# Kernel tuning notes

Hardware: AMD Instinct MI355X
Metric: run time of the kernel (lower is better)

Reference implementation:

```python
import jax, jax.numpy as jnp
import numpy as np

NUM_NODES = 100000
NUM_EDGES = 6400000


def setup_inputs() -> dict:
    key = jax.random.key(0)
    k1, k2 = jax.random.split(key)
    e = jax.random.normal(k1, (NUM_EDGES,), dtype=jnp.float32)
    edge_index = jax.random.randint(k2, (2, NUM_EDGES), 0, NUM_NODES, dtype=jnp.int64 if jax.config.jax_enable_x64 else jnp.int32)
    return {"e": e, "edge_index": edge_index, "num_nodes": NUM_NODES}


def reference(e, edge_index, num_nodes):
    # GAT edge softmax (no max-subtraction, matching the 'simple' variant)
    target_nodes = edge_index[1]                      # [E]
    exp_e = jnp.exp(e)                                # [E]
    sum_exp = jax.ops.segment_sum(exp_e, target_nodes, num_segments=num_nodes)  # [N]
    alpha = exp_e / (sum_exp[target_nodes] + 1e-16)   # gather + normalize
    return alpha
```

## Files before the change

kernel.cpp:

```cpp
#include <hip/hip_runtime.h>


#define CHUNK 36864
#define SCAT_THREADS 1024
#define ASSUMED_N 100000
#define SUMS_RESERVE (1u << 20)


__global__ __launch_bounds__(SCAT_THREADS)
void gat_scatter_chunked(const float* __restrict__ e,
                         const int* __restrict__ tgt,
                         const int* __restrict__ np,
                         float* __restrict__ partials,
                         int per, int E, int Cmax) {
    __shared__ float hist[CHUNK];
    const int n = *np;
    int C = (n + CHUNK - 1) / CHUNK;
    if (C > Cmax) C = Cmax;

    const int b = blockIdx.x;
    const int start = b * per;
    const int end = min(start + per, E);
    const int len = (end > start) ? (end - start) : 0;
    const int vlen = len & ~3;

    for (int c = 0; c < C; ++c) {
        const int base = c * CHUNK;

        for (int i = threadIdx.x; i < CHUNK; i += SCAT_THREADS) hist[i] = 0.0f;
        __syncthreads();

        for (int i = threadIdx.x * 4; i < vlen; i += SCAT_THREADS * 4) {
            const float4 ev = *reinterpret_cast<const float4*>(e + start + i);
            const int4  tv = *reinterpret_cast<const int4*>(tgt + start + i);
            int t;
            t = tv.x - base; if ((unsigned)t < (unsigned)CHUNK) atomicAdd(&hist[t], __expf(ev.x));
            t = tv.y - base; if ((unsigned)t < (unsigned)CHUNK) atomicAdd(&hist[t], __expf(ev.y));
            t = tv.z - base; if ((unsigned)t < (unsigned)CHUNK) atomicAdd(&hist[t], __expf(ev.z));
            t = tv.w - base; if ((unsigned)t < (unsigned)CHUNK) atomicAdd(&hist[t], __expf(ev.w));
        }
        for (int i = vlen + threadIdx.x; i < len; i += SCAT_THREADS) {
            int t = tgt[start + i] - base;
            if ((unsigned)t < (unsigned)CHUNK) atomicAdd(&hist[t], __expf(e[start + i]));
        }
        __syncthreads();

        float* dst = partials + ((size_t)b * Cmax + c) * CHUNK;
        for (int i = threadIdx.x; i < CHUNK; i += SCAT_THREADS) dst[i] = hist[i];
        __syncthreads();
    }
}

__global__ void gat_reduce(const float* __restrict__ partials,
                           const int* __restrict__ np,
                           float* __restrict__ sums,
                           int B, int CC ) {
    const int n = *np;
    const int gs = gridDim.x * blockDim.x;
    for (int nd = blockIdx.x * blockDim.x + threadIdx.x; nd < n; nd += gs) {
        if (nd >= CC) { sums[nd] = 0.0f; continue; }
        const float* p = partials + nd;
        float s0 = 0.f, s1 = 0.f, s2 = 0.f, s3 = 0.f;
        int b = 0;
        for (; b + 3 < B; b += 4) {
            s0 += p[(size_t)(b + 0) * CC];
            s1 += p[(size_t)(b + 1) * CC];
            s2 += p[(size_t)(b + 2) * CC];
            s3 += p[(size_t)(b + 3) * CC];
        }
        for (; b < B; ++b) s0 += p[(size_t)b * CC];
        sums[nd] = (s0 + s1) + (s2 + s3);
    }
}


__global__ void gat_zero_sums(float* __restrict__ sums,
                              const int* __restrict__ np) {
    const int n = *np;
    const int stride = gridDim.x * blockDim.x;
    for (int i = blockIdx.x * blockDim.x + threadIdx.x; i < n; i += stride)
        sums[i] = 0.0f;
}

__global__ void gat_exp_scatter(const float4* __restrict__ e4,
                                const int4* __restrict__ t4,
                                const float* __restrict__ e,
                                const int* __restrict__ tgt,
                                float* __restrict__ sums,
                                int n4, int E) {
    const int stride = gridDim.x * blockDim.x;
    int tid = blockIdx.x * blockDim.x + threadIdx.x;
    for (int i = tid; i < n4; i += stride) {
        float4 ev = e4[i];
        int4 tv = t4[i];
        atomicAdd(&sums[tv.x], __expf(ev.x));
        atomicAdd(&sums[tv.y], __expf(ev.y));
        atomicAdd(&sums[tv.z], __expf(ev.z));
        atomicAdd(&sums[tv.w], __expf(ev.w));
    }
    const int tail_base = n4 * 4;
    const int tail_n = E - tail_base;
    if (tid < tail_n)
        atomicAdd(&sums[tgt[tail_base + tid]], __expf(e[tail_base + tid]));
}


__global__ void gat_normalize(const float4* __restrict__ e4,
                              const int4* __restrict__ t4,
                              const float* __restrict__ e,
                              const int* __restrict__ tgt,
                              const float* __restrict__ sums,
                              float4* __restrict__ out4,
                              float* __restrict__ out,
                              int n4, int E) {
    const int stride = gridDim.x * blockDim.x;
    int tid = blockIdx.x * blockDim.x + threadIdx.x;
    for (int i = tid; i < n4; i += stride) {
        float4 ev = e4[i];
        int4 tv = t4[i];
        float4 r;
        r.x = __expf(ev.x) / (sums[tv.x] + 1e-16f);
        r.y = __expf(ev.y) / (sums[tv.y] + 1e-16f);
        r.z = __expf(ev.z) / (sums[tv.z] + 1e-16f);
        r.w = __expf(ev.w) / (sums[tv.w] + 1e-16f);
        out4[i] = r;
    }
    const int tail_base = n4 * 4;
    const int tail_n = E - tail_base;
    if (tid < tail_n) {
        int i = tail_base + tid;
        out[i] = __expf(e[i]) / (sums[tgt[i]] + 1e-16f);
    }
}

extern "C" void kernel_launch(void* const* d_in, const int* in_sizes, int n_in,
                              void* d_out, int out_size, void* d_ws, size_t ws_size,
                              hipStream_t stream) {
    const float* e = (const float*)d_in[0];
    const int* edge_index = (const int*)d_in[1];
    const int* num_nodes_p = (const int*)d_in[2];

    const int E = in_sizes[0];
    const int* tgt = edge_index + E;

    float* sums = (float*)d_ws;
    float* alpha = (float*)d_out;
    const int n4 = E / 4;

    const int Cmax = (ASSUMED_N + CHUNK - 1) / CHUNK;

    int B = 256;
    while (B >= 32 &&
           (SUMS_RESERVE + (size_t)B * Cmax * CHUNK * sizeof(float)) > ws_size)
        B >>= 1;

    const bool use_chunked =
        (SUMS_RESERVE + (size_t)B * Cmax * CHUNK * sizeof(float)) <= ws_size;

    if (use_chunked) {
        float* partials = (float*)((char*)d_ws + SUMS_RESERVE);
        const int per = (((E + B - 1) / B) + 3) & ~3;

        gat_scatter_chunked<<<B, SCAT_THREADS, 0, stream>>>(
            e, tgt, num_nodes_p, partials, per, E, Cmax);

        gat_reduce<<<512, 256, 0, stream>>>(
            partials, num_nodes_p, sums, B, Cmax * CHUNK);
    } else {
        gat_zero_sums<<<512, 256, 0, stream>>>(sums, num_nodes_p);
        int blocks = (n4 + 255) / 256;
        if (blocks > 2048) blocks = 2048;
        if (blocks < 1) blocks = 1;
        gat_exp_scatter<<<blocks, 256, 0, stream>>>(
            (const float4*)e, (const int4*)tgt, e, tgt, sums, n4, E);
    }

    {
        int blocks = (n4 + 255) / 256;
        if (blocks > 2048) blocks = 2048;
        if (blocks < 1) blocks = 1;
        gat_normalize<<<blocks, 256, 0, stream>>>(
            (const float4*)e, (const int4*)tgt, e, tgt, sums,
            (float4*)alpha, alpha, n4, E);
    }
}
```

Measured before the change: 113.0 us.

## Cache edge data in registers across chunks and store bf16 partial histograms

The chunked scatter kernel now loads each block's edges and their exponentials into registers once, instead of re-reading e and tgt from global memory for every node chunk. Partial per-block histograms are written as packed bf16 rather than fp32, which halves partial-sum traffic in both scatter and reduce. The reduce is vectorized over four nodes per thread. The bf16 rounding loses precision in the partial sums, and register caching sharply raises register pressure under a tighter launch bound.

```diff
diff --git a/kernel.cpp b/kernel.cpp
--- a/kernel.cpp
+++ b/kernel.cpp
@@ -3,73 +3,133 @@
 
 #define CHUNK 36864
 #define SCAT_THREADS 1024
+#define NPT 7
 #define ASSUMED_N 100000
 #define SUMS_RESERVE (1u << 20)
 
-
-__global__ __launch_bounds__(SCAT_THREADS)
-void gat_scatter_chunked(const float* __restrict__ e,
-                         const int* __restrict__ tgt,
-                         const int* __restrict__ np,
-                         float* __restrict__ partials,
-                         int per, int E, int Cmax) {
+__device__ __forceinline__ unsigned bf16rne(float f) {
+    unsigned u = __float_as_uint(f);
+    return (u + 0x7FFFu + ((u >> 16) & 1u)) >> 16;
+}
+__device__ __forceinline__ float bf16tof(unsigned short h) {
+    return __uint_as_float(((unsigned)h) << 16);
+}
+
+
+__global__ __launch_bounds__(SCAT_THREADS, 4)
+void gat_scatter_regcache(const float* __restrict__ e,
+                          const int* __restrict__ tgt,
+                          const int* __restrict__ np,
+                          unsigned short* __restrict__ partials,
+                          int per, int E, int Cmax) {
     __shared__ float hist[CHUNK];
     const int n = *np;
     int C = (n + CHUNK - 1) / CHUNK;
     if (C > Cmax) C = Cmax;
 
     const int b = blockIdx.x;
-    const int start = b * per;
-    const int end = min(start + per, E);
-    const int len = (end > start) ? (end - start) : 0;
-    const int vlen = len & ~3;
+    const int tid = threadIdx.x;
+    const long long start = (long long)b * per;
+
+    int nv = per >> 2;
+    long long rem = (long long)E - start;
+    if (rem < 0) rem = 0;
+    if ((long long)nv > (rem >> 2)) nv = (int)(rem >> 2);
+    const int tail_lo = nv * 4;
+    int tail_hi = per;
+    if ((long long)tail_hi > rem) tail_hi = (int)rem;
+
+    const float4* e4 = reinterpret_cast<const float4*>(e + start);
+    const int4*  t4 = reinterpret_cast<const int4*>(tgt + start);
+
+    float4 xv[NPT];
+    int4   iv[NPT];
+#pragma unroll
+    for (int i = 0; i < NPT; ++i) {
+        const int v = i * SCAT_THREADS + tid;
+        if (v < nv) {
+            const float4 ev = e4[v];
+            iv[i] = t4[v];
+            xv[i].x = __expf(ev.x); xv[i].y = __expf(ev.y);
+            xv[i].z = __expf(ev.z); xv[i].w = __expf(ev.w);
+        } else {
+            iv[i].x = iv[i].y = iv[i].z = iv[i].w = -1;
+            xv[i].x = xv[i].y = xv[i].z = xv[i].w = 0.0f;
+        }
+    }
 
     for (int c = 0; c < C; ++c) {
         const int base = c * CHUNK;
 
-        for (int i = threadIdx.x; i < CHUNK; i += SCAT_THREADS) hist[i] = 0.0f;
+        float4 z; z.x = z.y = z.z = z.w = 0.0f;
+        for (int j = tid; j < (CHUNK / 4); j += SCAT_THREADS)
+            reinterpret_cast<float4*>(hist)[j] = z;
         __syncthreads();
 
-        for (int i = threadIdx.x * 4; i < vlen; i += SCAT_THREADS * 4) {
-            const float4 ev = *reinterpret_cast<const float4*>(e + start + i);
-            const int4  tv = *reinterpret_cast<const int4*>(tgt + start + i);
+#pragma unroll
+        for (int i = 0; i < NPT; ++i) {
             int t;
-            t = tv.x - base; if ((unsigned)t < (unsigned)CHUNK) atomicAdd(&hist[t], __expf(ev.x));
-            t = tv.y - base; if ((unsigned)t < (unsigned)CHUNK) atomicAdd(&hist[t], __expf(ev.y));
-            t = tv.z - base; if ((unsigned)t < (unsigned)CHUNK) atomicAdd(&hist[t], __expf(ev.z));
-            t = tv.w - base; if ((unsigned)t < (unsigned)CHUNK) atomicAdd(&hist[t], __expf(ev.w));
-        }
-        for (int i = vlen + threadIdx.x; i < len; i += SCAT_THREADS) {
+            t = iv[i].x - base; if ((unsigned)t < (unsigned)CHUNK) atomicAdd(&hist[t], xv[i].x);
+            t = iv[i].y - base; if ((unsigned)t < (unsigned)CHUNK) atomicAdd(&hist[t], xv[i].y);
+            t = iv[i].z - base; if ((unsigned)t < (unsigned)CHUNK) atomicAdd(&hist[t], xv[i].z);
+            t = iv[i].w - base; if ((unsigned)t < (unsigned)CHUNK) atomicAdd(&hist[t], xv[i].w);
+        }
+        for (int i = tail_lo + tid; i < tail_hi; i += SCAT_THREADS) {
             int t = tgt[start + i] - base;
             if ((unsigned)t < (unsigned)CHUNK) atomicAdd(&hist[t], __expf(e[start + i]));
         }
         __syncthreads();
 
-        float* dst = partials + ((size_t)b * Cmax + c) * CHUNK;
-        for (int i = threadIdx.x; i < CHUNK; i += SCAT_THREADS) dst[i] = hist[i];
+        unsigned* dst = reinterpret_cast<unsigned*>(
+            partials + ((size_t)b * Cmax + c) * CHUNK);
+        const float2* h2 = reinterpret_cast<const float2*>(hist);
+        for (int j = tid; j < (CHUNK / 2); j += SCAT_THREADS) {
+            const float2 hv = h2[j];
+            dst[j] = bf16rne(hv.x) | (bf16rne(hv.y) << 16);
+        }
         __syncthreads();
     }
 }
 
-__global__ void gat_reduce(const float* __restrict__ partials,
-                           const int* __restrict__ np,
-                           float* __restrict__ sums,
-                           int B, int CC ) {
+
+__global__ void gat_reduce_bf16(const unsigned short* __restrict__ partials,
+                                const int* __restrict__ np,
+                                float* __restrict__ sums,
+                                int B, int CC ) {
     const int n = *np;
+    const int n4 = (n + 3) >> 2;
     const int gs = gridDim.x * blockDim.x;
-    for (int nd = blockIdx.x * blockDim.x + threadIdx.x; nd < n; nd += gs) {
-        if (nd >= CC) { sums[nd] = 0.0f; continue; }
-        const float* p = partials + nd;
+    for (int q = blockIdx.x * blockDim.x + threadIdx.x; q < n4; q += gs) {
+        const int nd = q * 4;
         float s0 = 0.f, s1 = 0.f, s2 = 0.f, s3 = 0.f;
-        int b = 0;
-        for (; b + 3 < B; b += 4) {
-            s0 += p[(size_t)(b + 0) * CC];
-            s1 += p[(size_t)(b + 1) * CC];
-            s2 += p[(size_t)(b + 2) * CC];
-            s3 += p[(size_t)(b + 3) * CC];
-        }
-        for (; b < B; ++b) s0 += p[(size_t)b * CC];
-        sums[nd] = (s0 + s1) + (s2 + s3);
+        float r0 = 0.f, r1 = 0.f, r2 = 0.f, r3 = 0.f;
+        if (nd < CC) {
+            const unsigned short* p = partials + nd;
+            int b = 0;
+            for (; b + 1 < B; b += 2) {
+                const ushort4 va = *reinterpret_cast<const ushort4*>(p + (size_t)b * CC);
+                const ushort4 vb = *reinterpret_cast<const ushort4*>(p + (size_t)(b + 1) * CC);
+                s0 += bf16tof(va.x); s1 += bf16tof(va.y);
+                s2 += bf16tof(va.z); s3 += bf16tof(va.w);
+                r0 += bf16tof(vb.x); r1 += bf16tof(vb.y);
+                r2 += bf16tof(vb.z); r3 += bf16tof(vb.w);
+            }
+            for (; b < B; ++b) {
+                const ushort4 v = *reinterpret_cast<const ushort4*>(p + (size_t)b * CC);
+                s0 += bf16tof(v.x); s1 += bf16tof(v.y);
+                s2 += bf16tof(v.z); s3 += bf16tof(v.w);
+            }
+        }
+        s0 += r0; s1 += r1; s2 += r2; s3 += r3;
+        if (nd + 4 <= n) {
+            float4 o; o.x = s0; o.y = s1; o.z = s2; o.w = s3;
+            *reinterpret_cast<float4*>(sums + nd) = o;
+        } else {
+            if (nd     < n) sums[nd]     = s0;
+            if (nd + 1 < n) sums[nd + 1] = s1;
+            if (nd + 2 < n) sums[nd + 2] = s2;
+            if (nd + 3 < n) sums[nd + 3] = s3;
+        }
     }
 }
 
@@ -145,42 +205,41 @@
 
     float* sums = (float*)d_ws;
     float* alpha = (float*)d_out;
-    const int n4 = E / 4;
+    const int n4e = E / 4;
 
     const int Cmax = (ASSUMED_N + CHUNK - 1) / CHUNK;
-
-    int B = 256;
-    while (B >= 32 &&
-           (SUMS_RESERVE + (size_t)B * Cmax * CHUNK * sizeof(float)) > ws_size)
-        B >>= 1;
-
-    const bool use_chunked =
-        (SUMS_RESERVE + (size_t)B * Cmax * CHUNK * sizeof(float)) <= ws_size;
+    const int B = 256;
+    const int per = (((E + B - 1) / B) + 3) & ~3;
+
+    bool use_chunked =
+        (SUMS_RESERVE + (size_t)B * Cmax * CHUNK * sizeof(unsigned short)) <= ws_size
+        && per <= NPT * SCAT_THREADS * 4;
 
     if (use_chunked) {
-        float* partials = (float*)((char*)d_ws + SUMS_RESERVE);
-        const int per = (((E + B - 1) / B) + 3) & ~3;
-
-        gat_scatter_chunked<<<B, SCAT_THREADS, 0, stream>>>(
+        unsigned short* partials =
+            (unsigned short*)((char*)d_ws + SUMS_RESERVE);
+
+        gat_scatter_regcache<<<B, SCAT_THREADS, 0, stream>>>(
             e, tgt, num_nodes_p, partials, per, E, Cmax);
 
-        gat_reduce<<<512, 256, 0, stream>>>(
+        const int rblocks = (ASSUMED_N / 4 + 255) / 256 + 1;
+        gat_reduce_bf16<<<rblocks, 256, 0, stream>>>(
             partials, num_nodes_p, sums, B, Cmax * CHUNK);
     } else {
         gat_zero_sums<<<512, 256, 0, stream>>>(sums, num_nodes_p);
-        int blocks = (n4 + 255) / 256;
+        int blocks = (n4e + 255) / 256;
         if (blocks > 2048) blocks = 2048;
         if (blocks < 1) blocks = 1;
         gat_exp_scatter<<<blocks, 256, 0, stream>>>(
-            (const float4*)e, (const int4*)tgt, e, tgt, sums, n4, E);
+            (const float4*)e, (const int4*)tgt, e, tgt, sums, n4e, E);
     }
 
     {
-        int blocks = (n4 + 255) / 256;
+        int blocks = (n4e + 255) / 256;
         if (blocks > 2048) blocks = 2048;
         if (blocks < 1) blocks = 1;
         gat_normalize<<<blocks, 256, 0, stream>>>(
             (const float4*)e, (const int4*)tgt, e, tgt, sums,
-            (float4*)alpha, alpha, n4, E);
-    }
-}
+            (float4*)alpha, alpha, n4e, E);
+    }
+}
```

Measured after the change: 126.2 us. +11.6%, slower.
